# Performance work log

Hardware: AMD Instinct MI355X
Metric: run time of the kernel (lower is better)

Reference implementation:

```python
import jax, jax.numpy as jnp
import numpy as np

GRID = 20          # visual_cortex_mask is an all-True GRID^3 volume -> S = 8000 active voxels
NUM_NEIGHBORS = 32
FEATURE_DIM = 512
NUM_HEADS = 8
BATCH = 4


def _knn_indices():
    # Coordinates of all active voxels in flat (active-order) indexing.
    zz, yy, xx = np.meshgrid(np.arange(GRID), np.arange(GRID), np.arange(GRID), indexing='ij')
    coords = np.stack([zz.ravel(), yy.ravel(), xx.ravel()], axis=1).astype(np.float32)  # [S,3]
    sq = (coords ** 2).sum(-1)
    d2 = sq[:, None] + sq[None, :] - 2.0 * (coords @ coords.T)  # squared distances [S,S]
    np.fill_diagonal(d2, np.inf)  # exclude self, mirrors nearest[:, 1:]
    nbr = np.argpartition(d2, NUM_NEIGHBORS - 1, axis=1)[:, :NUM_NEIGHBORS]
    return nbr.astype(np.int32)  # [S, K] positions in active-voxel order


def setup_inputs() -> dict:
    key = jax.random.key(0)
    k1, k2, k3, k4 = jax.random.split(key, 4)
    S = GRID ** 3
    x = jax.random.normal(k1, (BATCH, S, FEATURE_DIM), dtype=jnp.float32)
    scale = 0.02
    Wq = jax.random.normal(k2, (FEATURE_DIM, FEATURE_DIM), dtype=jnp.float32) * scale
    Wk = jax.random.normal(k3, (FEATURE_DIM, FEATURE_DIM), dtype=jnp.float32) * scale
    Wv = jax.random.normal(k4, (FEATURE_DIM, FEATURE_DIM), dtype=jnp.float32) * scale
    nbr = jnp.asarray(_knn_indices())
    return {"x": x, "Wq": Wq, "Wk": Wk, "Wv": Wv, "nbr": nbr}


def reference(x, Wq, Wk, Wv, nbr):
    B, S, F = x.shape
    H = NUM_HEADS
    Hd = F // H

    def proj(W):
        # nn.Linear(bias=False): x @ W.T, then split heads -> [B, H, S, Hd]
        return (x @ W.T).reshape(B, S, H, Hd).transpose(0, 2, 1, 3)

    q = proj(Wq)
    k = proj(Wk)
    v = proj(Wv)

    # Gather each query's fixed-size neighbor K/V set: [B, H, S, K, Hd].
    # Exactly equivalent to the flex_attention KNN mask (neighbor set == allowed kv set).
    kn = k[:, :, nbr, :]
    vn = v[:, :, nbr, :]

    scores = jnp.einsum('bhsd,bhskd->bhsk', q, kn) * (Hd ** -0.5)
    w = jax.nn.softmax(scores, axis=-1)
    out = jnp.einsum('bhsk,bhskd->bhsd', w, vn)  # [B, H, S, Hd]
    return out.transpose(0, 2, 1, 3).reshape(B, S, F)
```

## Files before the change

kernel.cpp:

```cpp
#include <hip/hip_runtime.h>
#include <cstddef>
#include <cstdint>

#define GRID_S 8000
#define FDIM 512
#define NHEAD 8
#define HD 64
#define KNN 32
#define NB 4
#define M_TOT (NB * GRID_S)

typedef __attribute__((ext_vector_type(8))) __bf16 bf16x8;
typedef __attribute__((ext_vector_type(4))) float f32x4;
typedef __attribute__((ext_vector_type(2))) float f32x2;
typedef __attribute__((ext_vector_type(2))) short short2v;

#if __has_builtin(__builtin_elementwise_fma)
#define FMA2(a,b,c) __builtin_elementwise_fma((a),(b),(c))
#else
#define FMA2(a,b,c) ((a)*(b)+(c))
#endif

#if __has_builtin(__builtin_amdgcn_fdot2_f32_bf16)
#define HAS_DOT2 1
#else
#define HAS_DOT2 0
#endif

__device__ inline ushort f2bf(float f) {
    uint32_t u = __builtin_bit_cast(uint32_t, f);
    uint32_t r = (u + 0x7fffu + ((u >> 16) & 1u)) >> 16;
    return (ushort)r;
}
__device__ inline f32x2 unpk(uint32_t u) {
    f32x2 r;
    r.x = __builtin_bit_cast(float, u << 16);
    r.y = __builtin_bit_cast(float, u & 0xffff0000u);
    return r;
}

#define NX4 (M_TOT * FDIM / 4)
#define NW4 (FDIM * FDIM / 4)

__global__ __launch_bounds__(256) void cvt_all(const float* __restrict__ x,
                                               const float* __restrict__ Wq,
                                               const float* __restrict__ Wk,
                                               const float* __restrict__ Wv,
                                               ushort* __restrict__ xb,
                                               ushort* __restrict__ wb) {
    int i = blockIdx.x * 256 + threadIdx.x;
    if (i < NX4) {
        float4 f = ((const float4*)x)[i];
        ushort4 o = { f2bf(f.x), f2bf(f.y), f2bf(f.z), f2bf(f.w) };
        ((ushort4*)xb)[i] = o;
        return;
    }
    i -= NX4;
    const int which = i >> 16;
    const int off = i & (NW4 - 1);
    const float* w = (which == 0) ? Wq : (which == 1) ? Wk : Wv;
    float4 f = ((const float4*)w)[off];
    ushort4 o = { f2bf(f.x), f2bf(f.y), f2bf(f.z), f2bf(f.w) };
    ((ushort4*)wb)[which * NW4 + off] = o;
}

#define TBM 128
#define TBN 128
#define TBK 32

__device__ inline void gload_lds16(const ushort* g, ushort* l) {
    __builtin_amdgcn_global_load_lds((const __attribute__((address_space(1))) uint32_t*)g,
                                     (__attribute__((address_space(3))) uint32_t*)l,
                                     16, 0, 0);
}

__global__ __launch_bounds__(256) void gemm_qkv(const ushort* __restrict__ A,
                                                const ushort* __restrict__ B,
                                                ushort* __restrict__ qo,
                                                ushort* __restrict__ ko,
                                                ushort* __restrict__ vo) {
    __shared__ ushort As[TBM * TBK];
    __shared__ ushort Bs[TBN * TBK];
    const int tid = threadIdx.x;
    const int wv = tid >> 6;
    const int lane = tid & 63;
    const int bm = blockIdx.x * TBM;
    const int bn = blockIdx.y * TBN;
    const int wr = (wv >> 1) * 64;
    const int wc = (wv & 1) * 64;
    f32x4 acc[4][4] = {};

    const int srow = wv * 32 + (lane >> 2);
    const int scol = (lane & 3) * 8;
    const int fr = lane & 15;
    const int fk = (lane >> 4) * 8;

    for (int k0 = 0; k0 < FDIM; k0 += TBK) {
        const ushort* ga = A + (size_t)(bm + srow) * FDIM + k0 + scol;
        const ushort* gb = B + (size_t)(bn + srow) * FDIM + k0 + scol;
        gload_lds16(ga,             &As[(wv * 32) * TBK]);
        gload_lds16(ga + 16 * FDIM, &As[(wv * 32 + 16) * TBK]);
        gload_lds16(gb,             &Bs[(wv * 32) * TBK]);
        gload_lds16(gb + 16 * FDIM, &Bs[(wv * 32 + 16) * TBK]);
        __syncthreads();

        bf16x8 af[4], bfr[4];
        #pragma unroll
        for (int i = 0; i < 4; ++i) {
            af[i]  = *(const bf16x8*)&As[(wr + i * 16 + fr) * TBK + fk];
            bfr[i] = *(const bf16x8*)&Bs[(wc + i * 16 + fr) * TBK + fk];
        }
        #pragma unroll
        for (int i = 0; i < 4; ++i)
            #pragma unroll
            for (int j = 0; j < 4; ++j)
                acc[i][j] = __builtin_amdgcn_mfma_f32_16x16x32_bf16(af[i], bfr[j], acc[i][j], 0, 0, 0);
        __syncthreads();
    }

    const int cr = (lane >> 4) * 4;
    const int cc = lane & 15;
    const int seg = blockIdx.y >> 2;
    const int cn = (blockIdx.y & 3) * TBN;
    ushort* dst = (seg == 0) ? qo : (seg == 1) ? ko : vo;
    const float scl = (seg == 0) ? 0.125f : 1.0f;
    #pragma unroll
    for (int i = 0; i < 4; ++i)
        #pragma unroll
        for (int j = 0; j < 4; ++j) {
            ushort* cp = dst + (size_t)(bm + wr + i * 16 + cr) * FDIM + cn + wc + j * 16 + cc;
            #pragma unroll
            for (int r = 0; r < 4; ++r)
                cp[(size_t)r * FDIM] = f2bf(acc[i][j][r] * scl);
        }
}

__global__ __launch_bounds__(256) void knn_attn5(const ushort* __restrict__ q,
                                                 const ushort* __restrict__ k,
                                                 const ushort* __restrict__ v,
                                                 const int* __restrict__ nbr,
                                                 float* __restrict__ out) {
    const int bid = blockIdx.x;
    const int base = ((bid & 7) * (M_TOT / 32) + (bid >> 3)) * 4;
    const int lane = threadIdx.x & 63;
    const int wv = threadIdx.x >> 6;
    const int bs = base + wv;
    const int b = bs / GRID_S;
    const int s = bs - b * GRID_S;
    const int* __restrict__ nrow = nbr + s * KNN;

    const uint4 qw = *(const uint4*)(q + (size_t)bs * FDIM + 8 * lane);
#if HAS_DOT2
    const short2v qs0 = __builtin_bit_cast(short2v, qw.x);
    const short2v qs1 = __builtin_bit_cast(short2v, qw.y);
    const short2v qs2 = __builtin_bit_cast(short2v, qw.z);
    const short2v qs3 = __builtin_bit_cast(short2v, qw.w);
#else
    const f32x2 q2[4] = { unpk(qw.x), unpk(qw.y), unpk(qw.z), unpk(qw.w) };
#endif

    const ushort* kb = k + (size_t)b * GRID_S * FDIM + 8 * lane;
    float sc[KNN];
    #pragma unroll
    for (int j = 0; j < KNN; ++j) {
        const uint4 kw = *(const uint4*)(kb + ((size_t)(uint32_t)nrow[j] << 9));
#if HAS_DOT2
        float p = __builtin_amdgcn_fdot2_f32_bf16(__builtin_bit_cast(short2v, kw.x), qs0, 0.f, false);
        p = __builtin_amdgcn_fdot2_f32_bf16(__builtin_bit_cast(short2v, kw.y), qs1, p, false);
        p = __builtin_amdgcn_fdot2_f32_bf16(__builtin_bit_cast(short2v, kw.z), qs2, p, false);
        p = __builtin_amdgcn_fdot2_f32_bf16(__builtin_bit_cast(short2v, kw.w), qs3, p, false);
#else
        f32x2 a2 = q2[0] * unpk(kw.x);
        a2 = FMA2(q2[1], unpk(kw.y), a2);
        a2 = FMA2(q2[2], unpk(kw.z), a2);
        a2 = FMA2(q2[3], unpk(kw.w), a2);
        float p = a2.x + a2.y;
#endif
        p += __shfl_xor(p, 1);
        p += __shfl_xor(p, 2);
        p += __shfl_xor(p, 4);
        sc[j] = p;
    }

    float mx = sc[0];
    #pragma unroll
    for (int j = 1; j < KNN; ++j) mx = fmaxf(mx, sc[j]);
    float sum = 0.f;
    #pragma unroll
    for (int j = 0; j < KNN; ++j) {
        sc[j] = __expf(sc[j] - mx);
        sum += sc[j];
    }
    const float inv = 1.0f / sum;

    const ushort* vb = v + (size_t)b * GRID_S * FDIM + 8 * lane;
    f32x2 acc[4] = {};
    #pragma unroll
    for (int j = 0; j < KNN; ++j) {
        const uint4 vw = *(const uint4*)(vb + ((size_t)(uint32_t)nrow[j] << 9));
        const f32x2 w2 = {sc[j], sc[j]};
        acc[0] = FMA2(w2, unpk(vw.x), acc[0]);
        acc[1] = FMA2(w2, unpk(vw.y), acc[1]);
        acc[2] = FMA2(w2, unpk(vw.z), acc[2]);
        acc[3] = FMA2(w2, unpk(vw.w), acc[3]);
    }
    const f32x2 inv2 = {inv, inv};
    #pragma unroll
    for (int r = 0; r < 4; ++r) acc[r] *= inv2;

    float* op = out + (size_t)bs * FDIM + 8 * lane;
    float4 o0 = {acc[0].x, acc[0].y, acc[1].x, acc[1].y};
    float4 o1 = {acc[2].x, acc[2].y, acc[3].x, acc[3].y};
    *(float4*)op = o0;
    *(float4*)(op + 4) = o1;
}

extern "C" void kernel_launch(void* const* d_in, const int* in_sizes, int n_in,
                              void* d_out, int out_size, void* d_ws, size_t ws_size,
                              hipStream_t stream) {
    const float* x  = (const float*)d_in[0];
    const float* Wq = (const float*)d_in[1];
    const float* Wk = (const float*)d_in[2];
    const float* Wv = (const float*)d_in[3];
    const int*   nbr = (const int*)d_in[4];
    float* out = (float*)d_out;

    const size_t m_elems = (size_t)M_TOT * FDIM;
    const size_t w_elems = (size_t)FDIM * FDIM;

    ushort* xb  = (ushort*)d_ws;
    ushort* wb  = xb + m_elems;
    ushort* kbf = wb + 3 * w_elems;
    ushort* vbf = kbf + m_elems;
    ushort* qbf = vbf + m_elems;

    cvt_all<<<(NX4 + 3 * NW4) / 256, 256, 0, stream>>>(x, Wq, Wk, Wv, xb, wb);

    dim3 grid(M_TOT / TBM, 3 * FDIM / TBN);
    gemm_qkv<<<grid, 256, 0, stream>>>(xb, wb, qbf, kbf, vbf);

    knn_attn5<<<M_TOT / 4, 256, 0, stream>>>(qbf, kbf, vbf, nbr, out);
}
```

Baseline: 214.2 us.

## Interleave K and V rows and use single-pass online softmax in KNN attention

The GEMM epilogue now writes K and V interleaved per token into one buffer, so each neighbor's K and V rows sit next to each other in memory. The attention kernel becomes a single pass with online softmax: it loads K and V for each neighbor together and rescales the accumulator only when the running max grows by more than a threshold, checked wave-wide. This removes the 32-entry score array and the second gather pass, which should reduce register pressure and improve locality. The cost is a data-dependent branch and extra exp calls per neighbor, and deferring the rescale with a threshold of 8 could hurt numerical accuracy.

```diff
diff --git a/kernel.cpp b/kernel.cpp
--- a/kernel.cpp
+++ b/kernel.cpp
@@ -77,8 +77,7 @@
 __global__ __launch_bounds__(256) void gemm_qkv(const ushort* __restrict__ A,
                                                 const ushort* __restrict__ B,
                                                 ushort* __restrict__ qo,
-                                                ushort* __restrict__ ko,
-                                                ushort* __restrict__ vo) {
+                                                ushort* __restrict__ kvo) {
     __shared__ ushort As[TBM * TBK];
     __shared__ ushort Bs[TBN * TBK];
     const int tid = threadIdx.x;
@@ -122,22 +121,32 @@
     const int cc = lane & 15;
     const int seg = blockIdx.y >> 2;
     const int cn = (blockIdx.y & 3) * TBN;
-    ushort* dst = (seg == 0) ? qo : (seg == 1) ? ko : vo;
-    const float scl = (seg == 0) ? 0.125f : 1.0f;
-    #pragma unroll
-    for (int i = 0; i < 4; ++i)
-        #pragma unroll
-        for (int j = 0; j < 4; ++j) {
-            ushort* cp = dst + (size_t)(bm + wr + i * 16 + cr) * FDIM + cn + wc + j * 16 + cc;
+    if (seg == 0) {
+        #pragma unroll
+        for (int i = 0; i < 4; ++i)
             #pragma unroll
-            for (int r = 0; r < 4; ++r)
-                cp[(size_t)r * FDIM] = f2bf(acc[i][j][r] * scl);
-        }
-}
-
-__global__ __launch_bounds__(256) void knn_attn5(const ushort* __restrict__ q,
-                                                 const ushort* __restrict__ k,
-                                                 const ushort* __restrict__ v,
+            for (int j = 0; j < 4; ++j) {
+                ushort* cp = qo + (size_t)(bm + wr + i * 16 + cr) * FDIM + cn + wc + j * 16 + cc;
+                #pragma unroll
+                for (int r = 0; r < 4; ++r)
+                    cp[(size_t)r * FDIM] = f2bf(acc[i][j][r] * 0.125f);
+            }
+    } else {
+        ushort* base = kvo + ((seg == 2) ? FDIM : 0);
+        #pragma unroll
+        for (int i = 0; i < 4; ++i)
+            #pragma unroll
+            for (int j = 0; j < 4; ++j) {
+                ushort* cp = base + (size_t)(bm + wr + i * 16 + cr) * (2 * FDIM) + cn + wc + j * 16 + cc;
+                #pragma unroll
+                for (int r = 0; r < 4; ++r)
+                    cp[(size_t)r * (2 * FDIM)] = f2bf(acc[i][j][r]);
+            }
+    }
+}
+
+__global__ __launch_bounds__(256) void knn_attn8(const ushort* __restrict__ q,
+                                                 const ushort* __restrict__ kv,
                                                  const int* __restrict__ nbr,
                                                  float* __restrict__ out) {
     const int bid = blockIdx.x;
@@ -159,51 +168,67 @@
     const f32x2 q2[4] = { unpk(qw.x), unpk(qw.y), unpk(qw.z), unpk(qw.w) };
 #endif
 
-    const ushort* kb = k + (size_t)b * GRID_S * FDIM + 8 * lane;
-    float sc[KNN];
+    const ushort* kvb = kv + (size_t)b * GRID_S * (2 * FDIM) + 8 * lane;
+
+#if HAS_DOT2
+#define SCORE1(kw, p)                                                                     \
+    p = __builtin_amdgcn_fdot2_f32_bf16(__builtin_bit_cast(short2v, kw.x), qs0, 0.f, false); \
+    p = __builtin_amdgcn_fdot2_f32_bf16(__builtin_bit_cast(short2v, kw.y), qs1, p, false);   \
+    p = __builtin_amdgcn_fdot2_f32_bf16(__builtin_bit_cast(short2v, kw.z), qs2, p, false);   \
+    p = __builtin_amdgcn_fdot2_f32_bf16(__builtin_bit_cast(short2v, kw.w), qs3, p, false);   \
+    p += __shfl_xor(p, 1); p += __shfl_xor(p, 2); p += __shfl_xor(p, 4);
+#else
+#define SCORE1(kw, p)                                                                     \
+    {                                                                                     \
+        f32x2 a2 = q2[0] * unpk(kw.x);                                                    \
+        a2 = FMA2(q2[1], unpk(kw.y), a2);                                                 \
+        a2 = FMA2(q2[2], unpk(kw.z), a2);                                                 \
+        a2 = FMA2(q2[3], unpk(kw.w), a2);                                                 \
+        p = a2.x + a2.y;                                                                  \
+    }                                                                                     \
+    p += __shfl_xor(p, 1); p += __shfl_xor(p, 2); p += __shfl_xor(p, 4);
+#endif
+
+    float m, sum;
+    f32x2 acc[4];
+    {
+        const ushort* rp = kvb + ((size_t)(uint32_t)nrow[0] << 10);
+        const uint4 kw = *(const uint4*)rp;
+        const uint4 vw = *(const uint4*)(rp + FDIM);
+        float p;
+        SCORE1(kw, p);
+        m = p;
+        sum = 1.f;
+        acc[0] = unpk(vw.x);
+        acc[1] = unpk(vw.y);
+        acc[2] = unpk(vw.z);
+        acc[3] = unpk(vw.w);
+    }
     #pragma unroll
-    for (int j = 0; j < KNN; ++j) {
-        const uint4 kw = *(const uint4*)(kb + ((size_t)(uint32_t)nrow[j] << 9));
-#if HAS_DOT2
-        float p = __builtin_amdgcn_fdot2_f32_bf16(__builtin_bit_cast(short2v, kw.x), qs0, 0.f, false);
-        p = __builtin_amdgcn_fdot2_f32_bf16(__builtin_bit_cast(short2v, kw.y), qs1, p, false);
-        p = __builtin_amdgcn_fdot2_f32_bf16(__builtin_bit_cast(short2v, kw.z), qs2, p, false);
-        p = __builtin_amdgcn_fdot2_f32_bf16(__builtin_bit_cast(short2v, kw.w), qs3, p, false);
-#else
-        f32x2 a2 = q2[0] * unpk(kw.x);
-        a2 = FMA2(q2[1], unpk(kw.y), a2);
-        a2 = FMA2(q2[2], unpk(kw.z), a2);
-        a2 = FMA2(q2[3], unpk(kw.w), a2);
-        float p = a2.x + a2.y;
-#endif
-        p += __shfl_xor(p, 1);
-        p += __shfl_xor(p, 2);
-        p += __shfl_xor(p, 4);
-        sc[j] = p;
-    }
-
-    float mx = sc[0];
-    #pragma unroll
-    for (int j = 1; j < KNN; ++j) mx = fmaxf(mx, sc[j]);
-    float sum = 0.f;
-    #pragma unroll
-    for (int j = 0; j < KNN; ++j) {
-        sc[j] = __expf(sc[j] - mx);
-        sum += sc[j];
-    }
-    const float inv = 1.0f / sum;
-
-    const ushort* vb = v + (size_t)b * GRID_S * FDIM + 8 * lane;
-    f32x2 acc[4] = {};
-    #pragma unroll
-    for (int j = 0; j < KNN; ++j) {
-        const uint4 vw = *(const uint4*)(vb + ((size_t)(uint32_t)nrow[j] << 9));
-        const f32x2 w2 = {sc[j], sc[j]};
+    for (int j = 1; j < KNN; ++j) {
+        const ushort* rp = kvb + ((size_t)(uint32_t)nrow[j] << 10);
+        const uint4 kw = *(const uint4*)rp;
+        const uint4 vw = *(const uint4*)(rp + FDIM);
+        float p;
+        SCORE1(kw, p);
+        if (__any(p - m > 8.f)) {
+            const float nm = fmaxf(m, p);
+            const float c = __expf(m - nm);
+            const f32x2 c2 = {c, c};
+            sum *= c;
+            acc[0] *= c2; acc[1] *= c2; acc[2] *= c2; acc[3] *= c2;
+            m = nm;
+        }
+        const float w = __expf(p - m);
+        sum += w;
+        const f32x2 w2 = {w, w};
         acc[0] = FMA2(w2, unpk(vw.x), acc[0]);
         acc[1] = FMA2(w2, unpk(vw.y), acc[1]);
         acc[2] = FMA2(w2, unpk(vw.z), acc[2]);
         acc[3] = FMA2(w2, unpk(vw.w), acc[3]);
     }
+
+    const float inv = 1.0f / sum;
     const f32x2 inv2 = {inv, inv};
     #pragma unroll
     for (int r = 0; r < 4; ++r) acc[r] *= inv2;
@@ -213,6 +238,7 @@
     float4 o1 = {acc[2].x, acc[2].y, acc[3].x, acc[3].y};
     *(float4*)op = o0;
     *(float4*)(op + 4) = o1;
+#undef SCORE1
 }
 
 extern "C" void kernel_launch(void* const* d_in, const int* in_sizes, int n_in,
@@ -230,14 +256,13 @@
 
     ushort* xb  = (ushort*)d_ws;
     ushort* wb  = xb + m_elems;
-    ushort* kbf = wb + 3 * w_elems;
-    ushort* vbf = kbf + m_elems;
-    ushort* qbf = vbf + m_elems;
+    ushort* kvb = wb + 3 * w_elems;
+    ushort* qbf = kvb + 2 * m_elems;
 
     cvt_all<<<(NX4 + 3 * NW4) / 256, 256, 0, stream>>>(x, Wq, Wk, Wv, xb, wb);
 
     dim3 grid(M_TOT / TBM, 3 * FDIM / TBN);
-    gemm_qkv<<<grid, 256, 0, stream>>>(xb, wb, qbf, kbf, vbf);
-
-    knn_attn5<<<M_TOT / 4, 256, 0, stream>>>(qbf, kbf, vbf, nbr, out);
-}
+    gemm_qkv<<<grid, 256, 0, stream>>>(xb, wb, qbf, kvb);
+
+    knn_attn8<<<M_TOT / 4, 256, 0, stream>>>(qbf, kvb, nbr, out);
+}
```

Measured after the change: 218.0 us. Within noise of the previous version (+1.8%).
